# Optimization experiments

Hardware: AMD Instinct MI355X
Metric: run time of the kernel (lower is better)

Reference implementation:

```python
import jax, jax.numpy as jnp
import numpy as np

P, C_IN, C_OUT, V = 3, 64, 32, 8192
EPS = 1e-5


def _layernorm(z, w, b):
    # normalized_shape = [C, 1, V]: normalize jointly over channel/temporal/node dims
    m = jnp.mean(z, axis=(1, 2, 3), keepdims=True)
    v = jnp.var(z, axis=(1, 2, 3), keepdims=True)
    return (z - m) * jax.lax.rsqrt(v + EPS) * w + b


def setup_inputs() -> dict:
    key = jax.random.key(0)
    ks = jax.random.split(key, 8)
    return {
        "x": jax.random.normal(ks[0], (1, C_IN, 1, V), jnp.float32),
        "A": jax.random.uniform(ks[1], (P, V, V), jnp.float32),
        "conv_w": jax.random.normal(ks[2], (C_OUT * P, C_IN), jnp.float32) * 0.1,
        "conv_b": jax.random.normal(ks[3], (C_OUT * P,), jnp.float32) * 0.1,
        "fifo_front": jax.random.normal(ks[4], (1, C_OUT, 1, V), jnp.float32),
        "acc_slot": jax.random.normal(ks[5], (1, C_OUT, 1, V), jnp.float32),
        "ln_w": jnp.ones((C_OUT, 1, V), jnp.float32),
        "ln_b": jnp.zeros((C_OUT, 1, V), jnp.float32),
        "res_w": jax.random.normal(ks[6], (C_OUT, C_IN), jnp.float32) * 0.1,
        "res_ln_w": jnp.ones((C_OUT, 1, V), jnp.float32),
        "res_ln_b": jnp.zeros((C_OUT, 1, V), jnp.float32),
    }


def reference(x, A, conv_w, conv_b, fifo_front, acc_slot, ln_w, ln_b, res_w, res_ln_w, res_ln_b):
    # residual branch: 1x1 conv (no bias) + LayerNorm
    res = _layernorm(jnp.einsum('oc,nclv->nolv', res_w, x), res_ln_w, res_ln_b)

    # main branch: 1x1 conv to P*C_out channels
    h = jnp.einsum('oc,nclv->nolv', conv_w, x) + conv_b[None, :, None, None]  # (1, P*C, 1, V)
    h = h.reshape(P, C_OUT, V)  # split into P partition chunks of C_OUT channels (N=1, L=1)

    # per-partition graph aggregation, summed over partitions
    y = jnp.einsum('pcv,pvw->cw', h, A)[None, :, None, :]  # (1, C, 1, V)

    # FIFO/accumulator step at fresh indices: acc += y; acc -= fifo_front; output = acc slot
    agg = acc_slot + y - fifo_front

    out = jax.nn.relu(_layernorm(agg, ln_w, ln_b))
    out = jax.nn.relu(out + res)  # residual add, then ReLU (Dropout is identity at inference)
    return out
```

## Files before the change

### kernel.cpp

```cpp
#include <hip/hip_runtime.h>
#include <hip/hip_bf16.h>


#define PP 3
#define CIN 64
#define COUT 32
#define VV 8192
#define EPSL 1e-5f
#define SPLITK 16

typedef short v8s __attribute__((ext_vector_type(8)));
typedef float v4f __attribute__((ext_vector_type(4)));

__device__ __forceinline__ void block_reduce2_store(float s1, float s2,
                                                    float* dst) {
  #pragma unroll
  for (int off = 32; off > 0; off >>= 1) {
    s1 += __shfl_down(s1, off, 64);
    s2 += __shfl_down(s2, off, 64);
  }
  __shared__ float r1[4], r2[4];
  int lane = threadIdx.x & 63, wv = threadIdx.x >> 6;
  if (lane == 0) { r1[wv] = s1; r2[wv] = s2; }
  __syncthreads();
  if (threadIdx.x == 0) {
    dst[0] = r1[0] + r1[1] + r1[2] + r1[3];
    dst[1] = r2[0] + r2[1] + r2[2] + r2[3];
  }
}

__global__ __launch_bounds__(256) void k1_conv(
    const float* __restrict__ x, const float* __restrict__ conv_w,
    const float* __restrict__ conv_b, const float* __restrict__ res_w,
    __hip_bfloat16* __restrict__ h, float* __restrict__ res,
    float* __restrict__ res_part) {
  int v = blockIdx.x * 256 + threadIdx.x;
  int og = blockIdx.y;
  float xr[CIN];
  #pragma unroll
  for (int c = 0; c < CIN; ++c) xr[c] = x[c * VV + v];

  if (og < 3) {
    for (int i = 0; i < 32; ++i) {
      int o = og * 32 + i;
      float acc = conv_b[o];
      #pragma unroll
      for (int c = 0; c < CIN; ++c) acc = fmaf(conv_w[o * CIN + c], xr[c], acc);
      h[o * VV + v] = __float2bfloat16(acc);
    }
  } else {
    float s1 = 0.f, s2 = 0.f;
    for (int o = 0; o < COUT; ++o) {
      float acc = 0.f;
      #pragma unroll
      for (int c = 0; c < CIN; ++c) acc = fmaf(res_w[o * CIN + c], xr[c], acc);
      res[o * VV + v] = acc;
      s1 += acc; s2 += acc * acc;
    }
    block_reduce2_store(s1, s2, &res_part[blockIdx.x * 2]);
  }
}

#define TN 128
#define KC 32
#define CHUNKS 48
#define PAIR_DW 260
#define PAIR_BYTES 1040
#define BUF_BYTES (16 * PAIR_BYTES)

__global__ __launch_bounds__(256) void k2_gemm(
    const float* __restrict__ A, const __hip_bfloat16* __restrict__ h,
    float* __restrict__ y_part) {
  __shared__ char lds_raw[3][BUF_BYTES];
  const int tid = threadIdx.x;
  const int wv = tid >> 6, lane = tid & 63;
  const int quad = lane >> 4, l15 = lane & 15;
  const int wbase = blockIdx.x * TN;
  const int kbase = blockIdx.y * (KC * CHUNKS);
  const int srow = lane >> 5;
  const int scol = (lane & 31) * 4;

  v4f acc[2][2] = {};

  auto stage = [&](char* buf, int chunk) {
    int k0 = kbase + chunk * KC;
    int p = k0 >> 13, v0 = k0 & (VV - 1);
    const float* Ap = A + ((size_t)p << 26);
    for (int pr = wv; pr < 16; pr += 4) {
      const float* gp = Ap + (size_t)(v0 + 2 * pr + srow) * VV + wbase + scol;
      void* lp = (void*)(buf + pr * PAIR_BYTES);
      __builtin_amdgcn_global_load_lds(
          (const __attribute__((address_space(1))) void*)gp,
          (__attribute__((address_space(3))) void*)lp, 16, 0, 0);
    }
  };

  {
    int p0 = kbase >> 13, v00 = kbase & (VV - 1);
    const __hip_bfloat16* hp0 = h + (size_t)(p0 * COUT + l15) * VV + v00 + quad * 8;
    v8s tmp0 = *(const v8s*)hp0;
    v8s tmp1 = *(const v8s*)(hp0 + 16 * VV);
    stage(lds_raw[0], 0);

    v8s hfr0 = tmp0, hfr1 = tmp1;

    for (int c = 0; c < CHUNKS; ++c) {
      v8s hn0 = hfr0, hn1 = hfr1;
      if (c + 1 < CHUNKS) {
        int kk = kbase + (c + 1) * KC;
        int p = kk >> 13, v0n = kk & (VV - 1);
        const __hip_bfloat16* hpn =
            h + (size_t)(p * COUT + l15) * VV + v0n + quad * 8;
        hn0 = *(const v8s*)hpn;
        hn1 = *(const v8s*)(hpn + 16 * VV);
        stage(lds_raw[(c + 1) % 3], c + 1);
        asm volatile("s_waitcnt vmcnt(6)" ::: "memory");
      } else {
        asm volatile("s_waitcnt vmcnt(0)" ::: "memory");
      }
      __builtin_amdgcn_s_barrier();
      asm volatile("" ::: "memory");

      const float* lf = (const float*)lds_raw[c % 3];

      #pragma unroll
      for (int nt = 0; nt < 2; ++nt) {
        int wl = wv * 32 + nt * 16 + l15;
        union { unsigned u[4]; v8s s; } bf;
        #pragma unroll
        for (int t = 0; t < 4; ++t) {
          int pr = quad * 4 + t;
          float f0 = lf[pr * PAIR_DW + wl];
          float f1 = lf[pr * PAIR_DW + 128 + wl];
          bf.u[t] = __builtin_amdgcn_perm(__float_as_uint(f1),
                                          __float_as_uint(f0), 0x07060302u);
        }
        acc[0][nt] = __builtin_amdgcn_mfma_f32_16x16x32_bf16(hfr0, bf.s, acc[0][nt], 0, 0, 0);
        acc[1][nt] = __builtin_amdgcn_mfma_f32_16x16x32_bf16(hfr1, bf.s, acc[1][nt], 0, 0, 0);
      }
      hfr0 = hn0; hfr1 = hn1;
    }
  }

  float* yp = y_part + (size_t)blockIdx.y * COUT * VV;
  #pragma unroll
  for (int mt = 0; mt < 2; ++mt)
    #pragma unroll
    for (int nt = 0; nt < 2; ++nt)
      #pragma unroll
      for (int r = 0; r < 4; ++r) {
        int crow = mt * 16 + quad * 4 + r;
        int w = wbase + wv * 32 + nt * 16 + l15;
        yp[(size_t)crow * VV + w] = acc[mt][nt][r];
      }
}

__global__ __launch_bounds__(256) void k3_agg(
    const float* __restrict__ acc_slot, const float* __restrict__ fifo,
    const float* __restrict__ y_part, float* __restrict__ agg,
    float* __restrict__ agg_part) {
  int i = blockIdx.x * 256 + threadIdx.x;
  float4 s = ((const float4*)y_part)[i];
  #pragma unroll
  for (int kb = 1; kb < SPLITK; ++kb) {
    float4 t = ((const float4*)(y_part + (size_t)kb * COUT * VV))[i];
    s.x += t.x; s.y += t.y; s.z += t.z; s.w += t.w;
  }
  float4 av = ((const float4*)acc_slot)[i];
  float4 fv = ((const float4*)fifo)[i];
  float4 g;
  g.x = av.x + s.x - fv.x;
  g.y = av.y + s.y - fv.y;
  g.z = av.z + s.z - fv.z;
  g.w = av.w + s.w - fv.w;
  ((float4*)agg)[i] = g;
  float s1 = g.x + g.y + g.z + g.w;
  float s2 = g.x * g.x + g.y * g.y + g.z * g.z + g.w * g.w;
  block_reduce2_store(s1, s2, &agg_part[blockIdx.x * 2]);
}

__global__ __launch_bounds__(256) void k4_final(
    const float* __restrict__ agg, const float* __restrict__ res,
    const float* __restrict__ ln_w, const float* __restrict__ ln_b,
    const float* __restrict__ res_ln_w, const float* __restrict__ res_ln_b,
    const float* __restrict__ res_part, const float* __restrict__ agg_part,
    float* __restrict__ out) {
  __shared__ float sf[4];
  if (threadIdx.x < 64) {
    int lane = threadIdx.x;
    float a1 = 0.f, a2 = 0.f;
    #pragma unroll
    for (int j = 0; j < 4; ++j) {
      a1 += agg_part[2 * (lane + 64 * j)];
      a2 += agg_part[2 * (lane + 64 * j) + 1];
    }
    float r1 = 0.f, r2 = 0.f;
    if (lane < 32) { r1 = res_part[2 * lane]; r2 = res_part[2 * lane + 1]; }
    #pragma unroll
    for (int off = 32; off > 0; off >>= 1) {
      a1 += __shfl_down(a1, off, 64);
      a2 += __shfl_down(a2, off, 64);
      r1 += __shfl_down(r1, off, 64);
      r2 += __shfl_down(r2, off, 64);
    }
    if (lane == 0) {
      const float inv_n = 1.0f / (COUT * VV);
      float mr = r1 * inv_n;
      float vr = r2 * inv_n - mr * mr;
      float ma = a1 * inv_n;
      float va = a2 * inv_n - ma * ma;
      sf[0] = mr; sf[1] = rsqrtf(vr + EPSL);
      sf[2] = ma; sf[3] = rsqrtf(va + EPSL);
    }
  }
  __syncthreads();
  const float mr = sf[0], rsr = sf[1], ma = sf[2], rsa = sf[3];

  int i = blockIdx.x * 256 + threadIdx.x;
  float4 g = ((const float4*)agg)[i];
  float4 r = ((const float4*)res)[i];
  float4 w1 = ((const float4*)ln_w)[i], b1 = ((const float4*)ln_b)[i];
  float4 w2 = ((const float4*)res_ln_w)[i], b2 = ((const float4*)res_ln_b)[i];
  float4 o;
  o.x = fmaxf(fmaxf((g.x - ma) * rsa * w1.x + b1.x, 0.f) + (r.x - mr) * rsr * w2.x + b2.x, 0.f);
  o.y = fmaxf(fmaxf((g.y - ma) * rsa * w1.y + b1.y, 0.f) + (r.y - mr) * rsr * w2.y + b2.y, 0.f);
  o.z = fmaxf(fmaxf((g.z - ma) * rsa * w1.z + b1.z, 0.f) + (r.z - mr) * rsr * w2.z + b2.z, 0.f);
  o.w = fmaxf(fmaxf((g.w - ma) * rsa * w1.w + b1.w, 0.f) + (r.w - mr) * rsr * w2.w + b2.w, 0.f);
  ((float4*)out)[i] = o;
}

extern "C" void kernel_launch(void* const* d_in, const int* in_sizes, int n_in,
                              void* d_out, int out_size, void* d_ws, size_t ws_size,
                              hipStream_t stream) {
  const float* x        = (const float*)d_in[0];
  const float* A        = (const float*)d_in[1];
  const float* conv_w   = (const float*)d_in[2];
  const float* conv_b   = (const float*)d_in[3];
  const float* fifo     = (const float*)d_in[4];
  const float* acc_slot = (const float*)d_in[5];
  const float* ln_w     = (const float*)d_in[6];
  const float* ln_b     = (const float*)d_in[7];
  const float* res_w    = (const float*)d_in[8];
  const float* res_ln_w = (const float*)d_in[9];
  const float* res_ln_b = (const float*)d_in[10];
  float* out = (float*)d_out;

  char* ws = (char*)d_ws;
  __hip_bfloat16* h  = (__hip_bfloat16*)ws;
  float* y_part   = (float*)(ws + 1572864);
  float* agg      = (float*)(ws + 18350080);
  float* res      = (float*)(ws + 19398656);
  float* res_part = (float*)(ws + 20447232);
  float* agg_part = (float*)(ws + 20447488);

  k1_conv<<<dim3(32, 4), 256, 0, stream>>>(x, conv_w, conv_b, res_w, h, res, res_part);
  k2_gemm<<<dim3(VV / TN, SPLITK), 256, 0, stream>>>(A, h, y_part);
  k3_agg<<<256, 256, 0, stream>>>(acc_slot, fifo, y_part, agg, agg_part);
  k4_final<<<256, 256, 0, stream>>>(agg, res, ln_w, ln_b, res_ln_w, res_ln_b,
                                    res_part, agg_part, out);
}
```

Before: 1.046 ms.

## Load A fragments directly from global memory instead of LDS-staged pipeline

Replaces the triple-buffered global_load_lds staging of A tiles, with its manual waitcnt and barrier pipelining, by per-thread direct global loads of A columns feeding the bf16 MFMA. Adds a launch bounds occupancy hint of 4 blocks per SM. This removes LDS traffic and block barriers but drops explicit prefetch overlap. Each lane now issues scalar 4-byte loads strided across rows, and latency hiding depends on occupancy and the compiler's scheduling.

```diff
diff --git a/kernel.cpp b/kernel.cpp
--- a/kernel.cpp
+++ b/kernel.cpp
@@ -64,82 +64,49 @@
 #define TN 128
 #define KC 32
 #define CHUNKS 48
-#define PAIR_DW 260
-#define PAIR_BYTES 1040
-#define BUF_BYTES (16 * PAIR_BYTES)
-
-__global__ __launch_bounds__(256) void k2_gemm(
+
+__global__ __launch_bounds__(256, 4) void k2_gemm(
     const float* __restrict__ A, const __hip_bfloat16* __restrict__ h,
     float* __restrict__ y_part) {
-  __shared__ char lds_raw[3][BUF_BYTES];
   const int tid = threadIdx.x;
   const int wv = tid >> 6, lane = tid & 63;
   const int quad = lane >> 4, l15 = lane & 15;
   const int wbase = blockIdx.x * TN;
   const int kbase = blockIdx.y * (KC * CHUNKS);
-  const int srow = lane >> 5;
-  const int scol = (lane & 31) * 4;
+  const int col0 = wbase + wv * 32 + l15;
 
   v4f acc[2][2] = {};
 
-  auto stage = [&](char* buf, int chunk) {
-    int k0 = kbase + chunk * KC;
-    int p = k0 >> 13, v0 = k0 & (VV - 1);
-    const float* Ap = A + ((size_t)p << 26);
-    for (int pr = wv; pr < 16; pr += 4) {
-      const float* gp = Ap + (size_t)(v0 + 2 * pr + srow) * VV + wbase + scol;
-      void* lp = (void*)(buf + pr * PAIR_BYTES);
-      __builtin_amdgcn_global_load_lds(
-          (const __attribute__((address_space(1))) void*)gp,
-          (__attribute__((address_space(3))) void*)lp, 16, 0, 0);
-    }
-  };
-
-  {
-    int p0 = kbase >> 13, v00 = kbase & (VV - 1);
-    const __hip_bfloat16* hp0 = h + (size_t)(p0 * COUT + l15) * VV + v00 + quad * 8;
-    v8s tmp0 = *(const v8s*)hp0;
-    v8s tmp1 = *(const v8s*)(hp0 + 16 * VV);
-    stage(lds_raw[0], 0);
-
-    v8s hfr0 = tmp0, hfr1 = tmp1;
-
-    for (int c = 0; c < CHUNKS; ++c) {
-      v8s hn0 = hfr0, hn1 = hfr1;
-      if (c + 1 < CHUNKS) {
-        int kk = kbase + (c + 1) * KC;
-        int p = kk >> 13, v0n = kk & (VV - 1);
-        const __hip_bfloat16* hpn =
-            h + (size_t)(p * COUT + l15) * VV + v0n + quad * 8;
-        hn0 = *(const v8s*)hpn;
-        hn1 = *(const v8s*)(hpn + 16 * VV);
-        stage(lds_raw[(c + 1) % 3], c + 1);
-        asm volatile("s_waitcnt vmcnt(6)" ::: "memory");
-      } else {
-        asm volatile("s_waitcnt vmcnt(0)" ::: "memory");
-      }
-      __builtin_amdgcn_s_barrier();
-      asm volatile("" ::: "memory");
-
-      const float* lf = (const float*)lds_raw[c % 3];
-
-      #pragma unroll
-      for (int nt = 0; nt < 2; ++nt) {
-        int wl = wv * 32 + nt * 16 + l15;
-        union { unsigned u[4]; v8s s; } bf;
-        #pragma unroll
-        for (int t = 0; t < 4; ++t) {
-          int pr = quad * 4 + t;
-          float f0 = lf[pr * PAIR_DW + wl];
-          float f1 = lf[pr * PAIR_DW + 128 + wl];
-          bf.u[t] = __builtin_amdgcn_perm(__float_as_uint(f1),
-                                          __float_as_uint(f0), 0x07060302u);
-        }
-        acc[0][nt] = __builtin_amdgcn_mfma_f32_16x16x32_bf16(hfr0, bf.s, acc[0][nt], 0, 0, 0);
-        acc[1][nt] = __builtin_amdgcn_mfma_f32_16x16x32_bf16(hfr1, bf.s, acc[1][nt], 0, 0, 0);
-      }
-      hfr0 = hn0; hfr1 = hn1;
-    }
+  for (int c = 0; c < CHUNKS; ++c) {
+    int kk = kbase + c * KC;
+    int p = kk >> 13, v0 = kk & (VV - 1);
+
+    const __hip_bfloat16* hp =
+        h + (size_t)(p * COUT + l15) * VV + v0 + quad * 8;
+    v8s hf0 = *(const v8s*)hp;
+    v8s hf1 = *(const v8s*)(hp + 16 * VV);
+
+    const float* Ap = A + ((size_t)p << 26) + (size_t)(v0 + quad * 8) * VV;
+    float a0[8], a1[8];
+    #pragma unroll
+    for (int j = 0; j < 8; ++j) {
+      a0[j] = Ap[(size_t)j * VV + col0];
+      a1[j] = Ap[(size_t)j * VV + col0 + 16];
+    }
+
+    union { unsigned u[4]; v8s s; } b0, b1;
+    #pragma unroll
+    for (int t = 0; t < 4; ++t) {
+      b0.u[t] = __builtin_amdgcn_perm(__float_as_uint(a0[2 * t + 1]),
+                                      __float_as_uint(a0[2 * t]), 0x07060302u);
+      b1.u[t] = __builtin_amdgcn_perm(__float_as_uint(a1[2 * t + 1]),
+                                      __float_as_uint(a1[2 * t]), 0x07060302u);
+    }
+
+    acc[0][0] = __builtin_amdgcn_mfma_f32_16x16x32_bf16(hf0, b0.s, acc[0][0], 0, 0, 0);
+    acc[1][0] = __builtin_amdgcn_mfma_f32_16x16x32_bf16(hf1, b0.s, acc[1][0], 0, 0, 0);
+    acc[0][1] = __builtin_amdgcn_mfma_f32_16x16x32_bf16(hf0, b1.s, acc[0][1], 0, 0, 0);
+    acc[1][1] = __builtin_amdgcn_mfma_f32_16x16x32_bf16(hf1, b1.s, acc[1][1], 0, 0, 0);
   }
 
   float* yp = y_part + (size_t)blockIdx.y * COUT * VV;
```

New measurement: 1.070 ms. 2.3% more time.
